# Kernel tuning notes

Measured on AMD Instinct MI355X. Metric: run time of the kernel, lower is better.

## Reference

```python
import jax, jax.numpy as jnp
import numpy as np

DIM = 512

def setup_inputs() -> dict:
    key = jax.random.key(0)
    ks = jax.random.split(key, 10)
    B, N, D = 8, 4096, DIM
    s = 1.0 / np.sqrt(D)
    return {
        "x": jax.random.normal(ks[0], (B, N, D), dtype=jnp.float32),
        "wq": jax.random.normal(ks[1], (D, D), dtype=jnp.float32) * s,
        "bq": jnp.zeros((D,), dtype=jnp.float32),
        "wk": jax.random.normal(ks[2], (D, D), dtype=jnp.float32) * s,
        "bk": jnp.zeros((D,), dtype=jnp.float32),
        "wp": jax.random.normal(ks[3], (D, D), dtype=jnp.float32) * s,
        "bp": jnp.zeros((D,), dtype=jnp.float32),
        "wf": jax.random.normal(ks[4], (D, D), dtype=jnp.float32) * s,
        "bf": jnp.zeros((D,), dtype=jnp.float32),
        "w_g": jax.random.normal(ks[5], (D, 1), dtype=jnp.float32),
    }

def reference(x, wq, bq, wk, bk, wp, bp, wf, bf, w_g):
    D = x.shape[-1]
    scale = D ** (-0.5)
    query = x @ wq + bq                      # [B,N,D]
    key_t = x @ wk + bk                      # [B,N,D]
    # l2 normalize along last dim (tf.math.l2_normalize uses eps=1e-12 via rsqrt of max(sum_sq, eps))
    def l2n(t):
        ss = jnp.sum(t * t, axis=-1, keepdims=True)
        return t * jax.lax.rsqrt(jnp.maximum(ss, 1e-12))
    query = l2n(query)
    key_t = l2n(key_t)
    query_weight = query @ w_g               # [B,N,1]
    scaled = query_weight * scale
    # Faithful to TF code: softmax over axis=-1 of a size-1 axis -> all ones
    attn = jax.nn.softmax(scaled, axis=-1)   # [B,N,1] == 1.0
    global_queries = jnp.sum(attn * query, axis=1)  # [B,D]
    gq = global_queries[:, None, :]          # broadcast over N (tile)
    out = (gq * key_t) @ wp + bp + query     # [B,N,D]
    out = out @ wf + bf
    return out
```

## Files before the change

### kernel.cpp

```cpp
#include <hip/hip_runtime.h>
#include <stdint.h>

typedef __bf16 bf16x8 __attribute__((ext_vector_type(8)));
typedef float floatx4 __attribute__((ext_vector_type(4)));
typedef unsigned short u16;
typedef u16 u16x8 __attribute__((ext_vector_type(8)));

__device__ __forceinline__ float bf2f(u16 u) {
    union { uint32_t i; float f; } v; v.i = ((uint32_t)u) << 16; return v.f;
}
__device__ __forceinline__ u16 f2bf(float f) {
    union { float f; uint32_t i; } v; v.f = f;
    uint32_t r = v.i + 0x7fffu + ((v.i >> 16) & 1u);
    return (u16)(r >> 16);
}

__device__ __forceinline__ void gload_lds16(const u16* g, u16* l) {
    __builtin_amdgcn_global_load_lds(
        (const __attribute__((address_space(1))) void*)g,
        (__attribute__((address_space(3))) void*)l,
        16, 0, 0);
}

#define BK 64

__global__ __launch_bounds__(512, 2) void gemm1_kernel(
    const u16* __restrict__ A,
    const u16* __restrict__ Bt,
    const float* __restrict__ bias,
    float* __restrict__ ssq_out,
    u16* __restrict__ C16)
{
    __shared__ __attribute__((aligned(16))) u16 lds[2 * 32768];
    const int tid  = threadIdx.x;
    const int wave = tid >> 6;
    const int lane = tid & 63;
    const int quad = lane >> 4;
    const int l16  = lane & 15;
    const int wm = wave >> 2, wn = wave & 3;

    const int gx   = gridDim.x;
    const int nwg  = gx * gridDim.y;
    const int wgid = blockIdx.y * gx + blockIdx.x;
    const int cpx  = nwg >> 3;
    const int swz  = (wgid & 7) * cpx + (wgid >> 3);
    const int row0 = (swz / gx) * 256;
    const int col0 = (swz % gx) * 256;

    floatx4 acc[8][4] = {};

    const int rsub = lane >> 3;
    const int ksub = ((lane & 7) ^ rsub) << 3;
    const u16* aptr[4]; const u16* bptr[4];
#pragma unroll
    for (int c = 0; c < 4; ++c) {
        const int cc = wave * 4 + c;
        aptr[c] = A  + (size_t)(row0 + cc * 8 + rsub) * 512 + ksub;
        bptr[c] = Bt + (size_t)(col0 + cc * 8 + rsub) * 512 + ksub;
    }
    const int NT = 8;

#define STAGE1(T, B)                                                          \
    {                                                                         \
        u16* dA_ = &lds[(B) * 32768];                                         \
        u16* dB_ = dA_ + 16384;                                               \
        const int kt_ = (T) * BK;                                             \
        _Pragma("unroll")                                                     \
        for (int c = 0; c < 4; ++c) {                                         \
            const int cc = wave * 4 + c;                                      \
            gload_lds16(aptr[c] + kt_, dA_ + cc * 512);                       \
            gload_lds16(bptr[c] + kt_, dB_ + cc * 512);                       \
        }                                                                     \
    }

    STAGE1(0, 0);
    STAGE1(1, 1);
    for (int t = 0; t < NT; ++t) {
        if (t + 1 < NT) asm volatile("s_waitcnt vmcnt(8)" ::: "memory");
        else            asm volatile("s_waitcnt vmcnt(0)" ::: "memory");
        __builtin_amdgcn_s_barrier();
        __builtin_amdgcn_sched_barrier(0);
        const u16* sA = &lds[(t & 1) * 32768];
        const u16* sB = sA + 16384;
#pragma unroll
        for (int ks = 0; ks < 2; ++ks) {
            const int pgo = (((ks * 4 + quad) ^ (l16 & 7)) << 3);
            bf16x8 bfr[4];
#pragma unroll
            for (int n = 0; n < 4; ++n)
                bfr[n] = *(const bf16x8*)&sB[(wn * 64 + n * 16 + l16) * 64 + pgo];
            __builtin_amdgcn_s_setprio(1);
#pragma unroll
            for (int m = 0; m < 8; ++m) {
                bf16x8 af = *(const bf16x8*)&sA[(wm * 128 + m * 16 + l16) * 64 + pgo];
#pragma unroll
                for (int n = 0; n < 4; ++n)
                    acc[m][n] = __builtin_amdgcn_mfma_f32_16x16x32_bf16(af, bfr[n], acc[m][n], 0, 0, 0);
            }
            __builtin_amdgcn_s_setprio(0);
        }
        __builtin_amdgcn_sched_barrier(0);
        asm volatile("" ::: "memory");
        __builtin_amdgcn_s_barrier();
        asm volatile("" ::: "memory");
        if (t + 2 < NT) STAGE1(t + 2, t & 1);
    }
#undef STAGE1

    u16* til = lds;
#pragma unroll
    for (int h = 0; h < 2; ++h) {
        __syncthreads();
        if (wm == h) {
            float bv[4];
#pragma unroll
            for (int n = 0; n < 4; ++n) bv[n] = bias[col0 + wn * 64 + n * 16 + l16];
#pragma unroll
            for (int m = 0; m < 8; ++m) {
                int rowl = m * 16 + quad * 4;
#pragma unroll
                for (int n = 0; n < 4; ++n) {
                    int tcol = wn * 64 + n * 16 + l16;
#pragma unroll
                    for (int t = 0; t < 4; ++t)
                        til[(rowl + t) * 264 + tcol] = f2bf(acc[m][n][t] + bv[n]);
                }
            }
        }
        __syncthreads();
        float ssl[8];
#pragma unroll
        for (int c = 0; c < 8; ++c) {
            int r  = c * 16 + (tid >> 5);
            int cu = (tid & 31) * 8;
            ushort4 lo = *(const ushort4*)&til[r * 264 + cu];
            ushort4 hi = *(const ushort4*)&til[r * 264 + cu + 4];
            u16x8 o;
            o[0] = lo.x; o[1] = lo.y; o[2] = lo.z; o[3] = lo.w;
            o[4] = hi.x; o[5] = hi.y; o[6] = hi.z; o[7] = hi.w;
            *(u16x8*)&C16[(size_t)(row0 + h * 128 + r) * 1024 + col0 + cu] = o;
            float ss = 0.f;
#pragma unroll
            for (int q2 = 0; q2 < 8; ++q2) { float f = bf2f(o[q2]); ss += f * f; }
            ssl[c] = ss;
        }
        float* so = ssq_out + (size_t)(col0 >> 9) * 32768 + row0 + h * 128;
#pragma unroll
        for (int c = 0; c < 8; ++c) {
            float s = ssl[c];
            s += __shfl_xor(s, 1);
            s += __shfl_xor(s, 2);
            s += __shfl_xor(s, 4);
            s += __shfl_xor(s, 8);
            s += __shfl_xor(s, 16);
            if ((lane & 31) == 0) atomicAdd(&so[c * 16 + (tid >> 5)], s);
        }
    }
}

__global__ __launch_bounds__(512, 2) void gemm_qk_kernel(
    const u16* __restrict__ A,
    const u16* __restrict__ BtF,
    const u16* __restrict__ BtPF,
    const float* __restrict__ bpf,
    const float* __restrict__ ssqQ,
    const float* __restrict__ ssqK,
    float* __restrict__ C32)
{
    __shared__ __attribute__((aligned(16))) u16 lds[2 * 32768];
    const int tid  = threadIdx.x;
    const int wave = tid >> 6;
    const int lane = tid & 63;
    const int quad = lane >> 4;
    const int l16  = lane & 15;
    const int wm = wave >> 2, wn = wave & 3;

    const int gx   = gridDim.x;
    const int nwg  = gx * gridDim.y;
    const int wgid = blockIdx.y * gx + blockIdx.x;
    const int cpx  = nwg >> 3;
    const int swz  = (wgid & 7) * cpx + (wgid >> 3);
    const int row0 = (swz / gx) * 256;
    const int col0 = (swz % gx) * 256;
    const int batch = row0 >> 12;

    floatx4 acc[8][4] = {};

    const int rsub = lane >> 3;
    const int ksub = ((lane & 7) ^ rsub) << 3;
    const u16* aptr[4]; const u16* bptrF[4]; const u16* bptrP[4];
    const u16* BP = BtPF + (size_t)batch * 262144;
#pragma unroll
    for (int c = 0; c < 4; ++c) {
        const int cc = wave * 4 + c;
        aptr[c]  = A   + (size_t)(row0 + cc * 8 + rsub) * 1024 + ksub;
        bptrF[c] = BtF + (size_t)(col0 + cc * 8 + rsub) * 512  + ksub;
        bptrP[c] = BP  + (size_t)(col0 + cc * 8 + rsub) * 512  + ksub;
    }
    const int NT = 16;

#define STAGEQ(T, B)                                                          \
    {                                                                         \
        u16* dA_ = &lds[(B) * 32768];                                         \
        u16* dB_ = dA_ + 16384;                                               \
        const int kt_ = (T) * BK;                                             \
        _Pragma("unroll")                                                     \
        for (int c = 0; c < 4; ++c) {                                         \
            const int cc = wave * 4 + c;                                      \
            gload_lds16(aptr[c] + kt_, dA_ + cc * 512);                       \
            const u16* bsrc_ = (kt_ < 512) ? (bptrF[c] + kt_)                 \
                                           : (bptrP[c] + (kt_ - 512));        \
            gload_lds16(bsrc_, dB_ + cc * 512);                               \
        }                                                                     \
    }

    STAGEQ(0, 0);
    STAGEQ(1, 1);
    for (int t = 0; t < NT; ++t) {
        if (t + 1 < NT) asm volatile("s_waitcnt vmcnt(8)" ::: "memory");
        else            asm volatile("s_waitcnt vmcnt(0)" ::: "memory");
        __builtin_amdgcn_s_barrier();
        __builtin_amdgcn_sched_barrier(0);
        const u16* sA = &lds[(t & 1) * 32768];
        const u16* sB = sA + 16384;
#pragma unroll
        for (int ks = 0; ks < 2; ++ks) {
            const int pgo = (((ks * 4 + quad) ^ (l16 & 7)) << 3);
            bf16x8 bfr[4];
#pragma unroll
            for (int n = 0; n < 4; ++n)
                bfr[n] = *(const bf16x8*)&sB[(wn * 64 + n * 16 + l16) * 64 + pgo];
            __builtin_amdgcn_s_setprio(1);
#pragma unroll
            for (int m = 0; m < 8; ++m) {
                bf16x8 af = *(const bf16x8*)&sA[(wm * 128 + m * 16 + l16) * 64 + pgo];
#pragma unroll
                for (int n = 0; n < 4; ++n)
                    acc[m][n] = __builtin_amdgcn_mfma_f32_16x16x32_bf16(af, bfr[n], acc[m][n], 0, 0, 0);
            }
            __builtin_amdgcn_s_setprio(0);
        }
        if (t == 7) {
#pragma unroll
            for (int m = 0; m < 8; ++m) {
                int rowb = row0 + wm * 128 + m * 16 + quad * 4;
                float4 q4 = *(const float4*)&ssqQ[rowb];
                float4 k4 = *(const float4*)&ssqK[rowb];
                float ratio[4];
                ratio[0] = rsqrtf(fmaxf(q4.x, 1e-12f)) / rsqrtf(fmaxf(k4.x, 1e-12f));
                ratio[1] = rsqrtf(fmaxf(q4.y, 1e-12f)) / rsqrtf(fmaxf(k4.y, 1e-12f));
                ratio[2] = rsqrtf(fmaxf(q4.z, 1e-12f)) / rsqrtf(fmaxf(k4.z, 1e-12f));
                ratio[3] = rsqrtf(fmaxf(q4.w, 1e-12f)) / rsqrtf(fmaxf(k4.w, 1e-12f));
#pragma unroll
                for (int n = 0; n < 4; ++n)
#pragma unroll
                    for (int tt = 0; tt < 4; ++tt)
                        acc[m][n][tt] *= ratio[tt];
            }
        }
        __builtin_amdgcn_sched_barrier(0);
        asm volatile("" ::: "memory");
        __builtin_amdgcn_s_barrier();
        asm volatile("" ::: "memory");
        if (t + 2 < NT) STAGEQ(t + 2, t & 1);
    }
#undef STAGEQ

    float* ftile = (float*)lds;
#pragma unroll
    for (int p = 0; p < 4; ++p) {
        __syncthreads();
        if (wm == (p >> 1)) {
            float bv[4];
#pragma unroll
            for (int n = 0; n < 4; ++n) bv[n] = bpf[col0 + wn * 64 + n * 16 + l16];
#pragma unroll
            for (int mi = 0; mi < 4; ++mi) {
                int m = (p & 1) * 4 + mi;
                int rowl = mi * 16 + quad * 4;
                int rowb = row0 + p * 64 + rowl;
                float4 k4 = *(const float4*)&ssqK[rowb];
                float rsk4[4];
                rsk4[0] = rsqrtf(fmaxf(k4.x, 1e-12f));
                rsk4[1] = rsqrtf(fmaxf(k4.y, 1e-12f));
                rsk4[2] = rsqrtf(fmaxf(k4.z, 1e-12f));
                rsk4[3] = rsqrtf(fmaxf(k4.w, 1e-12f));
#pragma unroll
                for (int n = 0; n < 4; ++n) {
                    int tcol = wn * 64 + n * 16 + l16;
#pragma unroll
                    for (int t = 0; t < 4; ++t)
                        ftile[(rowl + t) * 264 + tcol] = acc[m][n][t] * rsk4[t] + bv[n];
                }
            }
        }
        __syncthreads();
#pragma unroll
        for (int c = 0; c < 8; ++c) {
            int r  = c * 8 + wave;
            int cu = lane * 4;
            float4 v = *(const float4*)&ftile[r * 264 + cu];
            *(float4*)&C32[(size_t)(row0 + p * 64 + r) * 512 + col0 + cu] = v;
        }
    }
}

__global__ __launch_bounds__(256) void gemm128_kernel(
    const u16* __restrict__ A, int lda,
    const u16* __restrict__ Bt, int ldb,
    u16* __restrict__ C16, int ldc, int K)
{
    __shared__ __attribute__((aligned(16))) u16 lds[128 * 132];
    u16* lsA = lds;
    u16* lsB = lds + 128 * BK;
    const int tid  = threadIdx.x;
    const int wave = tid >> 6;
    const int lane = tid & 63;
    const int quad = lane >> 4;
    const int l16  = lane & 15;
    const int wm = wave >> 1, wn = wave & 1;

    const int gx   = gridDim.x;
    const int nwg  = gx * gridDim.y;
    const int wgid = blockIdx.y * gx + blockIdx.x;
    const int cpx  = nwg >> 3;
    const int swz  = (wgid & 7) * cpx + (wgid >> 3);
    const int row0 = (swz / gx) * 128;
    const int col0 = (swz % gx) * 128;

    floatx4 acc[4][4] = {};
    const int rsub = lane >> 3;
    const int ksub = ((lane & 7) ^ rsub) << 3;
    const u16* aptr[4]; const u16* bptr[4];
#pragma unroll
    for (int c = 0; c < 4; ++c) {
        const int cc = wave * 4 + c;
        aptr[c] = A  + (size_t)(row0 + cc * 8 + rsub) * lda + ksub;
        bptr[c] = Bt + (size_t)(col0 + cc * 8 + rsub) * ldb + ksub;
    }
    for (int kt = 0; kt < K; kt += BK) {
#pragma unroll
        for (int c = 0; c < 4; ++c) {
            const int cc = wave * 4 + c;
            gload_lds16(aptr[c] + kt, &lsA[cc * 512]);
            gload_lds16(bptr[c] + kt, &lsB[cc * 512]);
        }
        __syncthreads();
#pragma unroll
        for (int ks = 0; ks < 2; ++ks) {
            const int pgo = (((ks * 4 + quad) ^ (l16 & 7)) << 3);
            bf16x8 af[4], bfr[4];
#pragma unroll
            for (int i = 0; i < 4; ++i)
                af[i] = *(const bf16x8*)&lsA[(wm * 64 + i * 16 + l16) * BK + pgo];
#pragma unroll
            for (int j = 0; j < 4; ++j)
                bfr[j] = *(const bf16x8*)&lsB[(wn * 64 + j * 16 + l16) * BK + pgo];
#pragma unroll
            for (int i = 0; i < 4; ++i)
#pragma unroll
                for (int j = 0; j < 4; ++j)
                    acc[i][j] = __builtin_amdgcn_mfma_f32_16x16x32_bf16(af[i], bfr[j], acc[i][j], 0, 0, 0);
        }
        __syncthreads();
    }
#pragma unroll
    for (int j = 0; j < 4; ++j) {
        int tcol = wn * 64 + j * 16 + l16;
#pragma unroll
        for (int i = 0; i < 4; ++i) {
            int trow = wm * 64 + i * 16 + quad * 4;
#pragma unroll
            for (int t = 0; t < 4; ++t)
                lds[(trow + t) * 132 + tcol] = f2bf(acc[i][j][t]);
        }
    }
    __syncthreads();
#pragma unroll
    for (int c = 0; c < 8; ++c) {
        int r  = c * 16 + (tid >> 4);
        int cu = (tid & 15) * 8;
        ushort4 lo = *(const ushort4*)&lds[r * 132 + cu];
        ushort4 hi = *(const ushort4*)&lds[r * 132 + cu + 4];
        u16x8 o;
        o[0] = lo.x; o[1] = lo.y; o[2] = lo.z; o[3] = lo.w;
        o[4] = hi.x; o[5] = hi.y; o[6] = hi.z; o[7] = hi.w;
        *(u16x8*)&C16[(size_t)(row0 + r) * ldc + col0 + cu] = o;
    }
}

__global__ __launch_bounds__(256) void gsum_kernel(const u16* __restrict__ QK,
                                                   const float* __restrict__ ssqQ,
                                                   float* __restrict__ g)
{
    __shared__ float gtile[4][512];
    const int lane = threadIdx.x & 63;
    const int wave = threadIdx.x >> 6;
    const int row0 = blockIdx.x * 128 + wave * 32;
    const int batch = row0 >> 12;
    const int d = lane * 8;
    float gacc[8] = {};
    for (int rr = 0; rr < 32; ++rr) {
        int row = row0 + rr;
        float s = rsqrtf(fmaxf(ssqQ[row], 1e-12f));
        u16x8 q = *(const u16x8*)(QK + (size_t)row * 1024 + d);
#pragma unroll
        for (int i = 0; i < 8; ++i) gacc[i] += s * bf2f(q[i]);
    }
#pragma unroll
    for (int i = 0; i < 8; ++i) gtile[wave][d + i] = gacc[i];
    __syncthreads();
    int c2 = threadIdx.x * 2;
    float s0 = gtile[0][c2]     + gtile[1][c2]     + gtile[2][c2]     + gtile[3][c2];
    float s1 = gtile[0][c2 + 1] + gtile[1][c2 + 1] + gtile[2][c2 + 1] + gtile[3][c2 + 1];
    atomicAdd(&g[batch * 512 + c2], s0);
    atomicAdd(&g[batch * 512 + c2 + 1], s1);
}

__global__ __launch_bounds__(256) void scalePF_kernel(const u16* __restrict__ Pt,
                                                      const float* __restrict__ g,
                                                      u16* __restrict__ BtPF)
{
    size_t i8 = ((size_t)blockIdx.x * 256 + threadIdx.x) * 8;
    int b   = (int)(i8 >> 18);
    int rem = (int)(i8 & 262143);
    int kk  = rem & 511;
    u16x8 p = *(const u16x8*)(Pt + rem);
    float4 g0 = *(const float4*)(g + b * 512 + kk);
    float4 g1 = *(const float4*)(g + b * 512 + kk + 4);
    u16x8 o;
    o[0] = f2bf(bf2f(p[0]) * g0.x); o[1] = f2bf(bf2f(p[1]) * g0.y);
    o[2] = f2bf(bf2f(p[2]) * g0.z); o[3] = f2bf(bf2f(p[3]) * g0.w);
    o[4] = f2bf(bf2f(p[4]) * g1.x); o[5] = f2bf(bf2f(p[5]) * g1.y);
    o[6] = f2bf(bf2f(p[6]) * g1.z); o[7] = f2bf(bf2f(p[7]) * g1.w);
    *(u16x8*)(BtPF + (size_t)b * 262144 + rem) = o;
}

__global__ __launch_bounds__(512) void bpf_kernel(const float* __restrict__ wf,
                                                  const float* __restrict__ bp,
                                                  const float* __restrict__ bfv,
                                                  float* __restrict__ bpf)
{
    int n = threadIdx.x;
    int j0 = blockIdx.x * 64;
    float s = 0.f;
#pragma unroll 8
    for (int j = j0; j < j0 + 64; ++j) s += bp[j] * wf[(size_t)j * 512 + n];
    if (blockIdx.x == 0) s += bfv[n];
    atomicAdd(&bpf[n], s);
}

__global__ __launch_bounds__(256) void convert_x_kernel(const float* __restrict__ x, u16* __restrict__ xb)
{
    size_t i = ((size_t)blockIdx.x * 256 + threadIdx.x) * 4;
    float4 v = *(const float4*)(x + i);
    ushort4 o;
    o.x = f2bf(v.x); o.y = f2bf(v.y); o.z = f2bf(v.z); o.w = f2bf(v.w);
    *(ushort4*)(xb + i) = o;
}

__global__ __launch_bounds__(256) void convert_wp_kernel(const float* __restrict__ wp, u16* __restrict__ wpb)
{
    size_t i = ((size_t)blockIdx.x * 256 + threadIdx.x) * 4;
    float4 v = *(const float4*)(wp + i);
    ushort4 o;
    o.x = f2bf(v.x); o.y = f2bf(v.y); o.z = f2bf(v.z); o.w = f2bf(v.w);
    *(ushort4*)(wpb + i) = o;
}

__global__ __launch_bounds__(256) void transpose3_kernel(
    const float* __restrict__ w0, const float* __restrict__ w1, const float* __restrict__ w2,
    u16* __restrict__ d0, u16* __restrict__ d1, u16* __restrict__ d2)
{
    __shared__ u16 tile[32][34];
    const int which = blockIdx.x >> 8;
    const float* W = (which == 0) ? w0 : (which == 1) ? w1 : w2;
    u16* Bt = (which == 0) ? d0 : (which == 1) ? d1 : d2;
    const int bid = blockIdx.x & 255;
    const int tk = bid & 15;
    const int tn = bid >> 4;
    const int c  = threadIdx.x & 31;
    const int r0 = threadIdx.x >> 5;
#pragma unroll
    for (int i = 0; i < 4; ++i) {
        int r = r0 + i * 8;
        tile[r][c] = f2bf(W[(size_t)(tk * 32 + r) * 512 + tn * 32 + c]);
    }
    __syncthreads();
#pragma unroll
    for (int i = 0; i < 4; ++i) {
        int r = r0 + i * 8;
        Bt[(size_t)(tn * 32 + r) * 512 + tk * 32 + c] = tile[c][r];
    }
}

__global__ __launch_bounds__(256) void setup_kernel(const float* __restrict__ bq,
                                                    const float* __restrict__ bk,
                                                    float* __restrict__ biasQK,
                                                    float* __restrict__ g,
                                                    float* __restrict__ ssq,
                                                    float* __restrict__ bpf)
{
    int id = blockIdx.x * 256 + threadIdx.x;
    if (id < 1024) biasQK[id] = (id < 512) ? bq[id] : bk[id - 512];
    if (id < 4096) g[id] = 0.f;
    if (id < 512)  bpf[id] = 0.f;
    ssq[id] = 0.f;
}

extern "C" void kernel_launch(void* const* d_in, const int* in_sizes, int n_in,
                              void* d_out, int out_size, void* d_ws, size_t ws_size,
                              hipStream_t stream)
{
    const float* x  = (const float*)d_in[0];
    const float* wq = (const float*)d_in[1];
    const float* bq = (const float*)d_in[2];
    const float* wk = (const float*)d_in[3];
    const float* bk = (const float*)d_in[4];
    const float* wp = (const float*)d_in[5];
    const float* bp = (const float*)d_in[6];
    const float* wf = (const float*)d_in[7];
    const float* bf = (const float*)d_in[8];

    char* ws = (char*)d_ws;
    u16*   xb     = (u16*)(ws);
    u16*   QK     = (u16*)(ws + 33554432);
    u16*   Bt1    = (u16*)(ws + 100663296);
    u16*   BtF    = (u16*)(ws + 101711872);
    u16*   wpb    = (u16*)(ws + 102236160);
    u16*   Pt     = (u16*)(ws + 102760448);
    u16*   BtPF   = (u16*)(ws + 103284736);
    float* biasQK = (float*)(ws + 107479040);
    float* g      = (float*)(ws + 107483136);
    float* ssq    = (float*)(ws + 107499520);
    float* bpf    = (float*)(ws + 107761664);

    setup_kernel<<<256, 256, 0, stream>>>(bq, bk, biasQK, g, ssq, bpf);
    convert_x_kernel<<<16384, 256, 0, stream>>>(x, xb);
    transpose3_kernel<<<768, 256, 0, stream>>>(wq, wk, wf, Bt1, Bt1 + 512 * 512, BtF);
    convert_wp_kernel<<<256, 256, 0, stream>>>(wp, wpb);
    bpf_kernel<<<8, 512, 0, stream>>>(wf, bp, bf, bpf);
    gemm128_kernel<<<dim3(4, 4), 256, 0, stream>>>(BtF, 512, wpb, 512, Pt, 512, 512);

    gemm1_kernel<<<dim3(4, 128), 512, 0, stream>>>(xb, Bt1, biasQK, ssq, QK);
    gsum_kernel<<<256, 256, 0, stream>>>(QK, ssq, g);
    scalePF_kernel<<<1024, 256, 0, stream>>>(Pt, g, BtPF);
    gemm_qk_kernel<<<dim3(2, 128), 512, 0, stream>>>(QK, BtF, BtPF, bpf, ssq, ssq + 32768, (float*)d_out);
}
```

Measured before the change: 256.0 us.

## Merge prep kernels into one launch and fuse P GEMM with gsum

Combines the input conversion, weight transposes, wp conversion, bias copy and bias-projection kernels into a single prep kernel with block-range dispatch, and replaces the setup zeroing kernel with a memset. The small wf·wp GEMM is moved into the same launch as the global-query reduction as extra blocks, so it runs alongside that work. The aim is to cut launch count and inter-kernel gaps and to take the tiny GEMM off the critical path. The fused kernels have divergent block roles and share one LDS allocation sized for the larger role.

Result: faster. 244.3 us (-4.6%).

```diff
diff --git a/kernel.cpp b/kernel.cpp
--- a/kernel.cpp
+++ b/kernel.cpp
@@ -305,28 +305,48 @@
     }
 }
 
-__global__ __launch_bounds__(256) void gemm128_kernel(
-    const u16* __restrict__ A, int lda,
-    const u16* __restrict__ Bt, int ldb,
-    u16* __restrict__ C16, int ldc, int K)
+__global__ __launch_bounds__(256) void gsum_p_kernel(
+    const u16* __restrict__ QK, const float* __restrict__ ssqQ, float* __restrict__ g,
+    const u16* __restrict__ BtF, const u16* __restrict__ wpb, u16* __restrict__ Pt)
 {
-    __shared__ __attribute__((aligned(16))) u16 lds[128 * 132];
-    u16* lsA = lds;
-    u16* lsB = lds + 128 * BK;
+    __shared__ __attribute__((aligned(16))) char shmem[128 * 132 * 2];
     const int tid  = threadIdx.x;
+    const int lane = tid & 63;
     const int wave = tid >> 6;
-    const int lane = tid & 63;
+
+    if (blockIdx.x < 256) {
+        float (*gtile)[512] = (float(*)[512])shmem;
+        const int row0 = blockIdx.x * 128 + wave * 32;
+        const int batch = row0 >> 12;
+        const int d = lane * 8;
+        float gacc[8] = {};
+        for (int rr = 0; rr < 32; ++rr) {
+            int row = row0 + rr;
+            float s = rsqrtf(fmaxf(ssqQ[row], 1e-12f));
+            u16x8 q = *(const u16x8*)(QK + (size_t)row * 1024 + d);
+#pragma unroll
+            for (int i = 0; i < 8; ++i) gacc[i] += s * bf2f(q[i]);
+        }
+#pragma unroll
+        for (int i = 0; i < 8; ++i) gtile[wave][d + i] = gacc[i];
+        __syncthreads();
+        int c2 = tid * 2;
+        float s0 = gtile[0][c2]     + gtile[1][c2]     + gtile[2][c2]     + gtile[3][c2];
+        float s1 = gtile[0][c2 + 1] + gtile[1][c2 + 1] + gtile[2][c2 + 1] + gtile[3][c2 + 1];
+        atomicAdd(&g[batch * 512 + c2], s0);
+        atomicAdd(&g[batch * 512 + c2 + 1], s1);
+        return;
+    }
+
+    u16* lds  = (u16*)shmem;
+    u16* lsA  = lds;
+    u16* lsB  = lds + 128 * BK;
     const int quad = lane >> 4;
     const int l16  = lane & 15;
     const int wm = wave >> 1, wn = wave & 1;
-
-    const int gx   = gridDim.x;
-    const int nwg  = gx * gridDim.y;
-    const int wgid = blockIdx.y * gx + blockIdx.x;
-    const int cpx  = nwg >> 3;
-    const int swz  = (wgid & 7) * cpx + (wgid >> 3);
-    const int row0 = (swz / gx) * 128;
-    const int col0 = (swz % gx) * 128;
+    const int bid2 = blockIdx.x - 256;
+    const int row0 = (bid2 >> 2) * 128;
+    const int col0 = (bid2 & 3) * 128;
 
     floatx4 acc[4][4] = {};
     const int rsub = lane >> 3;
@@ -335,10 +355,10 @@
 #pragma unroll
     for (int c = 0; c < 4; ++c) {
         const int cc = wave * 4 + c;
-        aptr[c] = A  + (size_t)(row0 + cc * 8 + rsub) * lda + ksub;
-        bptr[c] = Bt + (size_t)(col0 + cc * 8 + rsub) * ldb + ksub;
-    }
-    for (int kt = 0; kt < K; kt += BK) {
+        aptr[c] = BtF + (size_t)(row0 + cc * 8 + rsub) * 512 + ksub;
+        bptr[c] = wpb + (size_t)(col0 + cc * 8 + rsub) * 512 + ksub;
+    }
+    for (int kt = 0; kt < 512; kt += BK) {
 #pragma unroll
         for (int c = 0; c < 4; ++c) {
             const int cc = wave * 4 + c;
@@ -385,36 +405,8 @@
         u16x8 o;
         o[0] = lo.x; o[1] = lo.y; o[2] = lo.z; o[3] = lo.w;
         o[4] = hi.x; o[5] = hi.y; o[6] = hi.z; o[7] = hi.w;
-        *(u16x8*)&C16[(size_t)(row0 + r) * ldc + col0 + cu] = o;
-    }
-}
-
-__global__ __launch_bounds__(256) void gsum_kernel(const u16* __restrict__ QK,
-                                                   const float* __restrict__ ssqQ,
-                                                   float* __restrict__ g)
-{
-    __shared__ float gtile[4][512];
-    const int lane = threadIdx.x & 63;
-    const int wave = threadIdx.x >> 6;
-    const int row0 = blockIdx.x * 128 + wave * 32;
-    const int batch = row0 >> 12;
-    const int d = lane * 8;
-    float gacc[8] = {};
-    for (int rr = 0; rr < 32; ++rr) {
-        int row = row0 + rr;
-        float s = rsqrtf(fmaxf(ssqQ[row], 1e-12f));
-        u16x8 q = *(const u16x8*)(QK + (size_t)row * 1024 + d);
-#pragma unroll
-        for (int i = 0; i < 8; ++i) gacc[i] += s * bf2f(q[i]);
-    }
-#pragma unroll
-    for (int i = 0; i < 8; ++i) gtile[wave][d + i] = gacc[i];
-    __syncthreads();
-    int c2 = threadIdx.x * 2;
-    float s0 = gtile[0][c2]     + gtile[1][c2]     + gtile[2][c2]     + gtile[3][c2];
-    float s1 = gtile[0][c2 + 1] + gtile[1][c2 + 1] + gtile[2][c2 + 1] + gtile[3][c2 + 1];
-    atomicAdd(&g[batch * 512 + c2], s0);
-    atomicAdd(&g[batch * 512 + c2 + 1], s1);
+        *(u16x8*)&Pt[(size_t)(row0 + r) * 512 + col0 + cu] = o;
+    }
 }
 
 __global__ __launch_bounds__(256) void scalePF_kernel(const u16* __restrict__ Pt,
@@ -436,76 +428,67 @@
     *(u16x8*)(BtPF + (size_t)b * 262144 + rem) = o;
 }
 
-__global__ __launch_bounds__(512) void bpf_kernel(const float* __restrict__ wf,
-                                                  const float* __restrict__ bp,
-                                                  const float* __restrict__ bfv,
-                                                  float* __restrict__ bpf)
-{
-    int n = threadIdx.x;
-    int j0 = blockIdx.x * 64;
-    float s = 0.f;
-#pragma unroll 8
-    for (int j = j0; j < j0 + 64; ++j) s += bp[j] * wf[(size_t)j * 512 + n];
-    if (blockIdx.x == 0) s += bfv[n];
-    atomicAdd(&bpf[n], s);
-}
-
-__global__ __launch_bounds__(256) void convert_x_kernel(const float* __restrict__ x, u16* __restrict__ xb)
-{
-    size_t i = ((size_t)blockIdx.x * 256 + threadIdx.x) * 4;
-    float4 v = *(const float4*)(x + i);
-    ushort4 o;
-    o.x = f2bf(v.x); o.y = f2bf(v.y); o.z = f2bf(v.z); o.w = f2bf(v.w);
-    *(ushort4*)(xb + i) = o;
-}
-
-__global__ __launch_bounds__(256) void convert_wp_kernel(const float* __restrict__ wp, u16* __restrict__ wpb)
-{
-    size_t i = ((size_t)blockIdx.x * 256 + threadIdx.x) * 4;
-    float4 v = *(const float4*)(wp + i);
-    ushort4 o;
-    o.x = f2bf(v.x); o.y = f2bf(v.y); o.z = f2bf(v.z); o.w = f2bf(v.w);
-    *(ushort4*)(wpb + i) = o;
-}
-
-__global__ __launch_bounds__(256) void transpose3_kernel(
-    const float* __restrict__ w0, const float* __restrict__ w1, const float* __restrict__ w2,
-    u16* __restrict__ d0, u16* __restrict__ d1, u16* __restrict__ d2)
+__global__ __launch_bounds__(256) void prep_kernel(
+    const float* __restrict__ x,  u16* __restrict__ xb,
+    const float* __restrict__ wq, const float* __restrict__ wk, const float* __restrict__ wf,
+    u16* __restrict__ Bt1, u16* __restrict__ BtF,
+    const float* __restrict__ wp, u16* __restrict__ wpb,
+    const float* __restrict__ bq, const float* __restrict__ bk, float* __restrict__ biasQK,
+    const float* __restrict__ bp, const float* __restrict__ bfv, float* __restrict__ bpf)
 {
     __shared__ u16 tile[32][34];
-    const int which = blockIdx.x >> 8;
-    const float* W = (which == 0) ? w0 : (which == 1) ? w1 : w2;
-    u16* Bt = (which == 0) ? d0 : (which == 1) ? d1 : d2;
-    const int bid = blockIdx.x & 255;
-    const int tk = bid & 15;
-    const int tn = bid >> 4;
-    const int c  = threadIdx.x & 31;
-    const int r0 = threadIdx.x >> 5;
-#pragma unroll
-    for (int i = 0; i < 4; ++i) {
-        int r = r0 + i * 8;
-        tile[r][c] = f2bf(W[(size_t)(tk * 32 + r) * 512 + tn * 32 + c]);
-    }
-    __syncthreads();
-#pragma unroll
-    for (int i = 0; i < 4; ++i) {
-        int r = r0 + i * 8;
-        Bt[(size_t)(tn * 32 + r) * 512 + tk * 32 + c] = tile[c][r];
-    }
-}
-
-__global__ __launch_bounds__(256) void setup_kernel(const float* __restrict__ bq,
-                                                    const float* __restrict__ bk,
-                                                    float* __restrict__ biasQK,
-                                                    float* __restrict__ g,
-                                                    float* __restrict__ ssq,
-                                                    float* __restrict__ bpf)
-{
-    int id = blockIdx.x * 256 + threadIdx.x;
-    if (id < 1024) biasQK[id] = (id < 512) ? bq[id] : bk[id - 512];
-    if (id < 4096) g[id] = 0.f;
-    if (id < 512)  bpf[id] = 0.f;
-    ssq[id] = 0.f;
+    const int bid = blockIdx.x;
+    const int tid = threadIdx.x;
+
+    if (bid < 16384) {
+        size_t i = ((size_t)bid * 256 + tid) * 4;
+        float4 v = *(const float4*)(x + i);
+        ushort4 o;
+        o.x = f2bf(v.x); o.y = f2bf(v.y); o.z = f2bf(v.z); o.w = f2bf(v.w);
+        *(ushort4*)(xb + i) = o;
+    } else if (bid < 17152) {
+        const int tb = bid - 16384;
+        const int which = tb >> 8;
+        const float* W = (which == 0) ? wq : (which == 1) ? wk : wf;
+        u16* Bt = (which == 0) ? Bt1 : (which == 1) ? (Bt1 + 512 * 512) : BtF;
+        const int b2 = tb & 255;
+        const int tk = b2 & 15;
+        const int tn = b2 >> 4;
+        const int c  = tid & 31;
+        const int r0 = tid >> 5;
+#pragma unroll
+        for (int i = 0; i < 4; ++i) {
+            int r = r0 + i * 8;
+            tile[r][c] = f2bf(W[(size_t)(tk * 32 + r) * 512 + tn * 32 + c]);
+        }
+        __syncthreads();
+#pragma unroll
+        for (int i = 0; i < 4; ++i) {
+            int r = r0 + i * 8;
+            Bt[(size_t)(tn * 32 + r) * 512 + tk * 32 + c] = tile[c][r];
+        }
+    } else if (bid < 17408) {
+        size_t i = ((size_t)(bid - 17152) * 256 + tid) * 4;
+        float4 v = *(const float4*)(wp + i);
+        ushort4 o;
+        o.x = f2bf(v.x); o.y = f2bf(v.y); o.z = f2bf(v.z); o.w = f2bf(v.w);
+        *(ushort4*)(wpb + i) = o;
+    } else if (bid < 17412) {
+        int id = (bid - 17408) * 256 + tid;
+        biasQK[id] = (id < 512) ? bq[id] : bk[id - 512];
+    } else {
+        const int bb = bid - 17412;
+        const int j0 = bb * 32;
+        float s0 = 0.f, s1 = 0.f;
+#pragma unroll 4
+        for (int j = j0; j < j0 + 32; ++j) {
+            s0 += bp[j] * wf[(size_t)j * 512 + tid];
+            s1 += bp[j] * wf[(size_t)j * 512 + tid + 256];
+        }
+        if (bb == 0) { s0 += bfv[tid]; s1 += bfv[tid + 256]; }
+        atomicAdd(&bpf[tid], s0);
+        atomicAdd(&bpf[tid + 256], s1);
+    }
 }
 
 extern "C" void kernel_launch(void* const* d_in, const int* in_sizes, int n_in,
@@ -535,15 +518,11 @@
     float* ssq    = (float*)(ws + 107499520);
     float* bpf    = (float*)(ws + 107761664);
 
-    setup_kernel<<<256, 256, 0, stream>>>(bq, bk, biasQK, g, ssq, bpf);
-    convert_x_kernel<<<16384, 256, 0, stream>>>(x, xb);
-    transpose3_kernel<<<768, 256, 0, stream>>>(wq, wk, wf, Bt1, Bt1 + 512 * 512, BtF);
-    convert_wp_kernel<<<256, 256, 0, stream>>>(wp, wpb);
-    bpf_kernel<<<8, 512, 0, stream>>>(wf, bp, bf, bpf);
-    gemm128_kernel<<<dim3(4, 4), 256, 0, stream>>>(BtF, 512, wpb, 512, Pt, 512, 512);
-
+    hipMemsetAsync(g, 0, 280576, stream);
+    prep_kernel<<<17428, 256, 0, stream>>>(x, xb, wq, wk, wf, Bt1, BtF, wp, wpb,
+                                           bq, bk, biasQK, bp, bf, bpf);
     gemm1_kernel<<<dim3(4, 128), 512, 0, stream>>>(xb, Bt1, biasQK, ssq, QK);
-    gsum_kernel<<<256, 256, 0, stream>>>(QK, ssq, g);
+    gsum_p_kernel<<<272, 256, 0, stream>>>(QK, ssq, g, BtF, wpb, Pt);
     scalePF_kernel<<<1024, 256, 0, stream>>>(Pt, g, BtPF);
     gemm_qk_kernel<<<dim3(2, 128), 512, 0, stream>>>(QK, BtF, BtPF, bpf, ssq, ssq + 32768, (float*)d_out);
 }
```
